# Performance work log

Measured on AMD Instinct MI355X. Metric: run time of the kernel, lower is better.

The kernel has to match this reference:

```python
import jax, jax.numpy as jnp
from jax import lax
import numpy as np

B, N, DIM = 2, 2048, 1024
HEADS, DIM_HEAD = 16, 64
KERNELS = (0, 3, 5, 7)
GROUPS = len(KERNELS)
HPG = HEADS // GROUPS          # heads per group = 4
CG = HPG * DIM_HEAD            # channels per group for depthwise conv = 256
INNER = HEADS * DIM_HEAD       # 1024


def _alibi_slopes(n):
    # power-of-2 branch of LearnedAlibiPosBias._get_slopes (n=4 here)
    start = 2.0 ** (-(2.0 ** -(np.log2(n) - 3)))
    return np.array([start * start ** i for i in range(n)], dtype=np.float32)


def setup_inputs() -> dict:
    key = jax.random.key(0)
    ks = jax.random.split(key, 24)
    d = {}
    d['x'] = jax.random.normal(ks[0], (B, N, DIM), jnp.float32)
    d['ln_gamma'] = jnp.ones((DIM,), jnp.float32)
    d['ln_beta'] = jnp.zeros((DIM,), jnp.float32)
    d['w_qkv'] = jax.random.normal(ks[1], (3 * INNER, DIM), jnp.float32) * 0.02
    i = 2
    for p in ('q', 'k', 'v'):
        for ksz in (3, 5, 7):
            d[f'dw{p}_w{ksz}'] = jax.random.normal(ks[i], (CG, 1, ksz), jnp.float32) * 0.1; i += 1
            d[f'dw{p}_b{ksz}'] = jax.random.normal(ks[i], (CG,), jnp.float32) * 0.02; i += 1
    # learned alibi slopes, initialized to the standard ALiBi values per group
    sl = _alibi_slopes(HPG).reshape(1, HPG, 1, 1)
    d['slopes'] = jnp.asarray(np.tile(sl, (GROUPS, 1, 1, 1)))
    d['w_out'] = jax.random.normal(ks[20], (DIM, INNER), jnp.float32) * 0.02
    return d


def _dw_causal_conv(xg, w, b, ksz):
    # xg: (B, CG, N); depthwise causal conv, left pad ksz-1
    xg = jnp.pad(xg, ((0, 0), (0, 0), (ksz - 1, 0)))
    out = lax.conv_general_dilated(xg, w, (1,), 'VALID',
                                   feature_group_count=CG,
                                   dimension_numbers=('NCH', 'OIH', 'NCH'))
    return out + b[None, :, None]


def _grouped_conv(t, w3, b3, w5, b5, w7, b7):
    # t: (B, INNER, N) channels laid out head-major; group g = channels [g*CG,(g+1)*CG)
    parts = [t[:, :CG]]  # group 0: kernel_size 0 -> Identity
    for i, (w, b, ksz) in enumerate(((w3, b3, 3), (w5, b5, 5), (w7, b7, 7))):
        parts.append(_dw_causal_conv(t[:, (i + 1) * CG:(i + 2) * CG], w, b, ksz))
    out = jnp.concatenate(parts, axis=1)                      # (B, INNER, N)
    out = out.reshape(B, HEADS, DIM_HEAD, N)
    return jnp.transpose(out, (0, 1, 3, 2))                   # (B, H, N, Dh)


def _forward(x, ln_gamma, ln_beta, w_qkv,
             dwq_w3, dwq_b3, dwq_w5, dwq_b5, dwq_w7, dwq_b7,
             dwk_w3, dwk_b3, dwk_w5, dwk_b5, dwk_w7, dwk_b7,
             dwv_w3, dwv_b3, dwv_w5, dwv_b5, dwv_w7, dwv_b7,
             slopes, w_out):
    scale = DIM_HEAD ** -0.5
    mu = jnp.mean(x, axis=-1, keepdims=True)
    var = jnp.var(x, axis=-1, keepdims=True)
    h = (x - mu) * lax.rsqrt(var + 1e-5) * ln_gamma + ln_beta   # (B, N, DIM)
    qkv = jnp.einsum('bnd,ed->ben', h, w_qkv)                   # (B, 3*INNER, N)
    q, k, v = jnp.split(qkv, 3, axis=1)
    q = _grouped_conv(q, dwq_w3, dwq_b3, dwq_w5, dwq_b5, dwq_w7, dwq_b7)
    k = _grouped_conv(k, dwk_w3, dwk_b3, dwk_w5, dwk_b5, dwk_w7, dwk_b7)
    v = _grouped_conv(v, dwv_w3, dwv_b3, dwv_w5, dwv_b5, dwv_w7, dwv_b7)
    sim = jnp.einsum('bhid,bhjd->bhij', q * scale, k)           # (B, H, N, N)
    idx = jnp.arange(N)
    dist = -jnp.abs(idx[None, :] - idx[:, None]).astype(sim.dtype)  # (N, N)
    bias = slopes.reshape(HEADS, 1, 1) * dist[None]             # (H, N, N)
    sim = sim + bias[None]
    causal = idx[None, :] > idx[:, None]                        # strictly future
    sim = jnp.where(causal[None, None], -jnp.finfo(sim.dtype).max, sim)
    attn = jax.nn.softmax(sim, axis=-1)
    out = jnp.einsum('bhij,bhjd->bhid', attn, v)                # (B, H, N, Dh)
    out = jnp.transpose(out, (0, 2, 1, 3)).reshape(B, N, INNER)
    return jnp.einsum('bne,de->bnd', out, w_out)


def reference(x, ln_gamma, ln_beta, w_qkv,
              dwq_w3, dwq_b3, dwq_w5, dwq_b5, dwq_w7, dwq_b7,
              dwk_w3, dwk_b3, dwk_w5, dwk_b5, dwk_w7, dwk_b7,
              dwv_w3, dwv_b3, dwv_w5, dwv_b5, dwv_w7, dwv_b7,
              slopes, w_out):
    return _forward(x, ln_gamma, ln_beta, w_qkv,
                    dwq_w3, dwq_b3, dwq_w5, dwq_b5, dwq_w7, dwq_b7,
                    dwk_w3, dwk_b3, dwk_w5, dwk_b5, dwk_w7, dwk_b7,
                    dwv_w3, dwv_b3, dwv_w5, dwv_b5, dwv_w7, dwv_b7,
                    slopes, w_out)
```

## Files before the change

kernel.cpp:

```cpp
#include <hip/hip_runtime.h>
#include <hip/hip_bf16.h>
#include <stdint.h>

typedef __bf16 bf8 __attribute__((ext_vector_type(8)));
typedef float  f4  __attribute__((ext_vector_type(4)));

constexpr int BATCH  = 2;
constexpr int SEQ    = 2048;
constexpr int DMODEL = 1024;
constexpr int NH     = 16;
constexpr int DHEAD  = 64;
constexpr int E3     = 3072;

static __device__ __forceinline__ f4 mfma16(bf8 a, bf8 b, f4 c){
  return __builtin_amdgcn_mfma_f32_16x16x32_bf16(a, b, c, 0, 0, 0);
}
static __device__ __forceinline__ uint32_t pack2(float a, float b){
  union { __bf16 h[2]; uint32_t u; } p;
  p.h[0] = (__bf16)a; p.h[1] = (__bf16)b;
  return p.u;
}
typedef const __attribute__((address_space(1))) uint32_t g_u32;
typedef __attribute__((address_space(3))) uint32_t l_u32;
static __device__ __forceinline__ void glds16(const __bf16* g, __bf16* l){
  __builtin_amdgcn_global_load_lds((g_u32*)g, (l_u32*)l, 16, 0, 0);
}

__global__ __launch_bounds__(256) void cvt_kernel(const float* __restrict__ s,
                                                  __bf16* __restrict__ d, int n){
  int i = (blockIdx.x * 256 + threadIdx.x) * 4;
  if(i < n){
    float4 v = *(const float4*)(s + i);
    __bf16 o[4] = {(__bf16)v.x, (__bf16)v.y, (__bf16)v.z, (__bf16)v.w};
    *(uint2*)(d + i) = *(const uint2*)o;
  }
}

__global__ __launch_bounds__(256) void prep_kernel(const float* __restrict__ x,
                                                   const float* __restrict__ gam,
                                                   const float* __restrict__ bet,
                                                   __bf16* __restrict__ h,
                                                   const float* __restrict__ wq,
                                                   __bf16* __restrict__ wqb){
  int bid = blockIdx.x;
  int tid = threadIdx.x;
  if(bid >= BATCH*SEQ){
    int i = ((bid - BATCH*SEQ) * 256 + tid) * 4;
    float4 v = *(const float4*)(wq + i);
    __bf16 o[4] = {(__bf16)v.x, (__bf16)v.y, (__bf16)v.z, (__bf16)v.w};
    *(uint2*)(wqb + i) = *(const uint2*)o;
    return;
  }
  int row = bid;
  const float* xr = x + (size_t)row * DMODEL;
  float4 v = *(const float4*)(xr + tid*4);
  float s = v.x + v.y + v.z + v.w;
  float ss = v.x*v.x + v.y*v.y + v.z*v.z + v.w*v.w;
#pragma unroll
  for(int m=1;m<64;m<<=1){ s += __shfl_xor(s, m); ss += __shfl_xor(ss, m); }
  __shared__ float sm[8];
  int wid = tid >> 6;
  if((tid & 63) == 0){ sm[wid] = s; sm[4+wid] = ss; }
  __syncthreads();
  s  = sm[0]+sm[1]+sm[2]+sm[3];
  ss = sm[4]+sm[5]+sm[6]+sm[7];
  float mu  = s * (1.f/DMODEL);
  float var = ss * (1.f/DMODEL) - mu*mu;
  float r = rsqrtf(var + 1e-5f);
  float4 g = *(const float4*)(gam + tid*4);
  float4 bb = *(const float4*)(bet + tid*4);
  __bf16 o[4] = { (__bf16)((v.x-mu)*r*g.x + bb.x), (__bf16)((v.y-mu)*r*g.y + bb.y),
                  (__bf16)((v.z-mu)*r*g.z + bb.z), (__bf16)((v.w-mu)*r*g.w + bb.w) };
  *(uint2*)(h + (size_t)row*DMODEL + tid*4) = *(uint2*)o;
}

template<typename CT>
__global__ __launch_bounds__(256) void gemm_nt(const __bf16* __restrict__ A,
                                               const __bf16* __restrict__ Bm,
                                               CT* __restrict__ C,
                                               int M, int Ncols, int K){
  __shared__ __align__(16) __bf16 sm[2*128*32];
  __bf16* As = sm;
  __bf16* Bs = sm + 128*32;
  int m0 = blockIdx.y * 128, n0 = blockIdx.x * 128;
  int tid = threadIdx.x;
  int lane = tid & 63, wid = tid >> 6;
  int quad = lane >> 4, l15 = lane & 15;
  int wm = (wid >> 1) * 64, wn = (wid & 1) * 64;
  f4 acc[4][4] = {};
  int r0 = wid*32 + (lane >> 2);
  int cofs = (lane & 3) * 8;
  const __bf16* ag = A  + (size_t)(m0 + r0) * K + cofs;
  const __bf16* bg = Bm + (size_t)(n0 + r0) * K + cofs;
  __bf16* asb0 = &As[(wid*32)*32];
  __bf16* asb1 = &As[(wid*32+16)*32];
  __bf16* bsb0 = &Bs[(wid*32)*32];
  __bf16* bsb1 = &Bs[(wid*32+16)*32];
  const size_t rowskip = (size_t)16 * K;
  for(int k0 = 0; k0 < K; k0 += 32){
    __syncthreads();
    glds16(ag + k0,           asb0);
    glds16(ag + rowskip + k0, asb1);
    glds16(bg + k0,           bsb0);
    glds16(bg + rowskip + k0, bsb1);
    __syncthreads();
    bf8 af[4], bfr[4];
#pragma unroll
    for(int i=0;i<4;i++){
      af[i]  = *(const bf8*)&As[(wm + i*16 + l15)*32 + quad*8];
      bfr[i] = *(const bf8*)&Bs[(wn + i*16 + l15)*32 + quad*8];
    }
#pragma unroll
    for(int mi=0;mi<4;mi++)
#pragma unroll
      for(int ni=0;ni<4;ni++)
        acc[mi][ni] = mfma16(af[mi], bfr[ni], acc[mi][ni]);
  }
  if constexpr (sizeof(CT) == 2){
    uint32_t* sp = (uint32_t*)sm;
#pragma unroll
    for(int qq=0; qq<4; qq++){
      __syncthreads();
      if((wid>>1) == (qq>>1)){
        int mi0 = (qq & 1) * 2;
#pragma unroll
        for(int mm=0; mm<2; mm++){
          int mi = mi0 + mm;
#pragma unroll
          for(int ni=0; ni<4; ni++)
#pragma unroll
            for(int r=0; r<4; r++){
              int lr = (mi - mi0)*16 + quad*4 + r;
              sm[lr*136 + wn + ni*16 + l15] = (__bf16)acc[mi][ni][r];
            }
        }
      }
      __syncthreads();
#pragma unroll
      for(int it=0; it<2; it++){
        int idx = it*256 + tid;
        int row = idx >> 4;
        int ck  = idx & 15;
        uint32_t o0 = sp[row*68 + ck*4 + 0];
        uint32_t o1 = sp[row*68 + ck*4 + 1];
        uint32_t o2 = sp[row*68 + ck*4 + 2];
        uint32_t o3 = sp[row*68 + ck*4 + 3];
        uint4 v = {o0, o1, o2, o3};
        *(uint4*)(C + (size_t)(m0 + qq*32 + row)*Ncols + n0 + ck*8) = v;
      }
    }
  } else {
#pragma unroll
    for(int mi=0;mi<4;mi++)
#pragma unroll
      for(int ni=0;ni<4;ni++)
#pragma unroll
        for(int r=0;r<4;r++){
          int row = m0 + wm + mi*16 + quad*4 + r;
          int col = n0 + wn + ni*16 + l15;
          C[(size_t)row*Ncols + col] = (CT)acc[mi][ni][r];
        }
  }
}

template<typename CT>
__global__ __launch_bounds__(256) void gemm_nt64(const __bf16* __restrict__ A,
                                                 const __bf16* __restrict__ Bm,
                                                 CT* __restrict__ C,
                                                 int M, int Ncols, int K){
  __shared__ __align__(16) __bf16 smb[(128+64)*32];
  __bf16* As = smb;
  __bf16* Bs = smb + 128*32;
  int m0 = blockIdx.y * 128, n0 = blockIdx.x * 64;
  int tid = threadIdx.x;
  int lane = tid & 63, wid = tid >> 6;
  int quad = lane >> 4, l15 = lane & 15;
  int wm = wid * 32;
  f4 acc[2][4] = {};
  int ra = wid*32 + (lane >> 2);
  int rb = wid*16 + (lane >> 2);
  int cofs = (lane & 3) * 8;
  const __bf16* ag = A  + (size_t)(m0 + ra) * K + cofs;
  const __bf16* bg = Bm + (size_t)(n0 + rb) * K + cofs;
  __bf16* asb0 = &As[(wid*32)*32];
  __bf16* asb1 = &As[(wid*32+16)*32];
  __bf16* bsb  = &Bs[(wid*16)*32];
  const size_t rowskip = (size_t)16 * K;
  for(int k0 = 0; k0 < K; k0 += 32){
    __syncthreads();
    glds16(ag + k0,           asb0);
    glds16(ag + rowskip + k0, asb1);
    glds16(bg + k0,           bsb);
    __syncthreads();
    bf8 af[2], bfr[4];
#pragma unroll
    for(int i=0;i<2;i++)
      af[i]  = *(const bf8*)&As[(wm + i*16 + l15)*32 + quad*8];
#pragma unroll
    for(int i=0;i<4;i++)
      bfr[i] = *(const bf8*)&Bs[(i*16 + l15)*32 + quad*8];
#pragma unroll
    for(int mi=0;mi<2;mi++)
#pragma unroll
      for(int ni=0;ni<4;ni++)
        acc[mi][ni] = mfma16(af[mi], bfr[ni], acc[mi][ni]);
  }
  if constexpr (sizeof(CT) == 4){
    float* sp = (float*)smb;
#pragma unroll
    for(int qq=0; qq<4; qq++){
      __syncthreads();
      if(wid == qq){
#pragma unroll
        for(int mi=0; mi<2; mi++)
#pragma unroll
          for(int ni=0; ni<4; ni++)
#pragma unroll
            for(int r=0; r<4; r++){
              int lr = mi*16 + quad*4 + r;
              sp[lr*68 + ni*16 + l15] = acc[mi][ni][r];
            }
      }
      __syncthreads();
#pragma unroll
      for(int it=0; it<2; it++){
        int idx = it*256 + tid;
        int row = idx >> 4;
        int ck  = idx & 15;
        float4 v = { sp[row*68 + ck*4 + 0], sp[row*68 + ck*4 + 1],
                     sp[row*68 + ck*4 + 2], sp[row*68 + ck*4 + 3] };
        *(float4*)(C + (size_t)(m0 + qq*32 + row)*Ncols + n0 + ck*4) = v;
      }
    }
  } else {
#pragma unroll
    for(int mi=0;mi<2;mi++)
#pragma unroll
      for(int ni=0;ni<4;ni++)
#pragma unroll
        for(int r=0;r<4;r++){
          int row = m0 + wm + mi*16 + quad*4 + r;
          int col = n0 + ni*16 + l15;
          C[(size_t)row*Ncols + col] = (CT)acc[mi][ni][r];
        }
  }
}

__global__ __launch_bounds__(256) void conv_kernel(const __bf16* __restrict__ qkv,
    __bf16* __restrict__ qo, __bf16* __restrict__ ko, __bf16* __restrict__ vt,
    const float* qw3,const float* qb3,const float* qw5,const float* qb5,const float* qw7,const float* qb7,
    const float* kw3,const float* kb3,const float* kw5,const float* kb5,const float* kw7,const float* kb7,
    const float* vw3,const float* vb3,const float* vw5,const float* vb5,const float* vw7,const float* vb7){
  __shared__ __align__(16) __bf16 tile[72*256];
  int nc = blockIdx.x;
  int ec = blockIdx.y;
  int b  = blockIdx.z;
  int tid = threadIdx.x;
  int n0 = nc * 64;
  {
    int rrow = tid >> 5;
    int ccol = (tid & 31) * 8;
    const __bf16* src = qkv + (size_t)b*SEQ*E3 + ec*256 + ccol;
#pragma unroll
    for(int p=0;p<9;p++){
      int row = p*8 + rrow;
      int n = n0 - 8 + row;
      uint4 v = {0u,0u,0u,0u};
      if(n >= 0) v = *(const uint4*)(src + (size_t)n*E3);
      *(uint4*)&tile[row*256 + ccol] = v;
    }
  }
  __syncthreads();
  int e = ec*256 + tid;
  int p  = e >> 10;
  int c  = e & 1023;
  int g  = c >> 8;
  int cg = c & 255;
  int hh = c >> 6;
  int dh = c & 63;
  const float* W[9]  = {qw3,qw5,qw7,kw3,kw5,kw7,vw3,vw5,vw7};
  const float* Bp[9] = {qb3,qb5,qb7,kb3,kb5,kb7,vb3,vb5,vb7};
  int ksz = (g==0)?0:((g==1)?3:((g==2)?5:7));
  float w[7] = {0,0,0,0,0,0,0};
  float bias = 0.f;
  if(g > 0){
    const float* wp = W[p*3 + g - 1];
    const float* bp = Bp[p*3 + g - 1];
    for(int t=0;t<ksz;t++) w[t] = wp[cg*ksz + t];
    bias = bp[cg];
  }
  float xh[6];
#pragma unroll
  for(int i=0;i<6;i++) xh[i] = (float)tile[(2+i)*256 + tid];
  if(p == 2){
    uint32_t vout[32];
#pragma unroll
    for(int blk=0; blk<8; blk++){
      __bf16 tmp[8];
#pragma unroll
      for(int u=0;u<8;u++){
        int dn = blk*8 + u;
        float cur = (float)tile[(8+dn)*256 + tid];
        float o;
        if(ksz == 0)      o = cur;
        else if(ksz == 3) o = w[0]*xh[4] + w[1]*xh[5] + w[2]*cur + bias;
        else if(ksz == 5) o = w[0]*xh[2] + w[1]*xh[3] + w[2]*xh[4] + w[3]*xh[5] + w[4]*cur + bias;
        else              o = w[0]*xh[0] + w[1]*xh[1] + w[2]*xh[2] + w[3]*xh[3] + w[4]*xh[4] + w[5]*xh[5] + w[6]*cur + bias;
        xh[0]=xh[1]; xh[1]=xh[2]; xh[2]=xh[3]; xh[3]=xh[4]; xh[4]=xh[5]; xh[5]=cur;
        tmp[u] = (__bf16)o;
      }
#pragma unroll
      for(int j=0;j<4;j++) vout[blk*4 + j] = ((const uint32_t*)tmp)[j];
    }
    __syncthreads();
    uint32_t* ot = (uint32_t*)tile;
#pragma unroll
    for(int j=0;j<32;j++) ot[tid*33 + j] = vout[j];
    __syncthreads();
#pragma unroll
    for(int it=0; it<8; it++){
      int idx = it*256 + tid;
      int ch  = idx >> 3;
      int ncq = idx & 7;
      uint32_t a0 = ot[ch*33 + ncq*4 + 0];
      uint32_t a1 = ot[ch*33 + ncq*4 + 1];
      uint32_t a2 = ot[ch*33 + ncq*4 + 2];
      uint32_t a3 = ot[ch*33 + ncq*4 + 3];
      uint4 val = {a0, a1, a2, a3};
      int hh2 = (ec & 3)*4 + (ch >> 6);
      int dh2 = ch & 63;
      *(uint4*)(vt + ((size_t)((b*NH + hh2)*DHEAD + dh2))*SEQ + n0 + ncq*8) = val;
    }
  } else {
    __bf16* outp = (p==0) ? qo : ko;
    __bf16* op = outp + ((size_t)(b*NH + hh)*SEQ)*DHEAD + dh;
#pragma unroll 4
    for(int dn=0; dn<64; dn++){
      float cur = (float)tile[(8+dn)*256 + tid];
      float o;
      if(ksz == 0)      o = cur;
      else if(ksz == 3) o = w[0]*xh[4] + w[1]*xh[5] + w[2]*cur + bias;
      else if(ksz == 5) o = w[0]*xh[2] + w[1]*xh[3] + w[2]*xh[4] + w[3]*xh[5] + w[4]*cur + bias;
      else              o = w[0]*xh[0] + w[1]*xh[1] + w[2]*xh[2] + w[3]*xh[3] + w[4]*xh[4] + w[5]*xh[5] + w[6]*cur + bias;
      xh[0]=xh[1]; xh[1]=xh[2]; xh[2]=xh[3]; xh[3]=xh[4]; xh[4]=xh[5]; xh[5]=cur;
      op[(size_t)(n0+dn)*DHEAD] = (__bf16)o;
    }
  }
}

__global__ __launch_bounds__(256, 2) void attn_kernel(const __bf16* __restrict__ Qin,
                                                      const __bf16* __restrict__ Kin,
                                                      const __bf16* __restrict__ Vtin,
                                                      const float* __restrict__ slopes,
                                                      __bf16* __restrict__ Oout){
  __shared__ __align__(16) __bf16 Ks[2][128*64];
  __shared__ __align__(16) __bf16 Vts[2][64*128];
  __shared__ __align__(16) __bf16 Ps[4][16*72];
  __shared__ float Al[4][16];
  int bid = blockIdx.x;
  int pr = bid >> 5;
  int by = (bid & 7) + ((bid >> 3) & 3) * 8;
  int b  = by >> 4, hh = by & 15;
  int tid = threadIdx.x, lane = tid & 63, w = tid >> 6;
  int quad = lane >> 4, l15 = lane & 15;
  const __bf16* qb  = Qin  + (size_t)by * SEQ * DHEAD;
  const __bf16* kb  = Kin  + (size_t)by * SEQ * DHEAD;
  const __bf16* vtb = Vtin + (size_t)by * DHEAD * SEQ;
  const float L2E = 1.4426950408889634f;
  float slope = slopes[hh];
  const float c1 = 0.125f * L2E;
  float c2 = slope * L2E;
  float c2_64 = c2 * 64.f;
  float cjb[16];
#pragma unroll
  for(int jt=0;jt<4;jt++)
#pragma unroll
    for(int r=0;r<4;r++)
      cjb[jt*4+r] = c2 * (float)(jt*16 + quad*4 + r);

  int sxq0 = ((quad     ^ (l15 & 7)) << 3);
  int sxq1 = (((quad+4) ^ (l15 & 7)) << 3);

  const __bf16* ksrc = kb + (size_t)(lane>>3)*DHEAD + ((lane&7) ^ ((lane>>3)&7))*8;
  const __bf16* vsrc[4];
#pragma unroll
  for(int u=0;u<4;u++){
    int g = w*4 + u;
    int vrow = g*4 + (lane>>4);
    vsrc[u] = vtb + (size_t)vrow*SEQ + (((lane&15) ^ (vrow&15)) * 8);
  }

  for(int ph=0; ph<2; ph++){
    int qi = ph ? (31 - pr) : pr;
    int q0 = qi * 64;
    int nst = (qi >> 1) + 1;
    int i0 = q0 + w*16;
    int i  = i0 + l15;
    bf8 aq0 = *(const bf8*)(qb + (size_t)i*DHEAD + quad*8);
    bf8 aq1 = *(const bf8*)(qb + (size_t)i*DHEAD + 32 + quad*8);
    f4 oacc[4] = {};
    float l_ = 0.f;
#pragma unroll
    for(int u=0;u<4;u++){
      int g = w*4 + u;
      glds16(ksrc + (size_t)g*8*DHEAD, &Ks[0][g*512]);
      glds16(vsrc[u],                  &Vts[0][g*512]);
    }
    __syncthreads();
    int cur = 0;
    for(int t=0; t<nst; t++){
      int j0 = t*128;
      bool pf = (t+1) < nst;
      if(pf){
        int nb = cur ^ 1;
#pragma unroll
        for(int u=0;u<4;u++){
          int g = w*4 + u;
          glds16(ksrc + (size_t)((t+1)*128 + g*8)*DHEAD, &Ks[nb][g*512]);
          glds16(vsrc[u] + (t+1)*128,                    &Vts[nb][g*512]);
        }
      }
      const __bf16* KsC  = Ks[cur];
      const __bf16* VtsC = Vts[cur];
      f4 s[8] = {};
      __builtin_amdgcn_s_setprio(1);
#pragma unroll
      for(int jt=0;jt<8;jt++){
        bf8 ak0 = *(const bf8*)&KsC[(jt*16+l15)*64 + sxq0];
        bf8 ak1 = *(const bf8*)&KsC[(jt*16+l15)*64 + sxq1];
        s[jt] = mfma16(ak0, aq0, s[jt]);
        s[jt] = mfma16(ak1, aq1, s[jt]);
      }
      __builtin_amdgcn_s_setprio(0);
      float lsum = 0.f;
      bool masked = (t == nst-1);
      float cdi = c2 * (float)(i - j0) + 8.0f;
#pragma unroll
      for(int h=0;h<2;h++){
        bf8 bv[2][4];
#pragma unroll
        for(int jj=0;jj<2;jj++){
          int jk = h*2 + jj;
#pragma unroll
          for(int nd=0;nd<4;nd++)
            bv[jj][nd] = *(const bf8*)&VtsC[(nd*16+l15)*128 + (((jk*4+quad) ^ l15) << 3)];
        }
        float sv[4][4];
        if(!masked){
#pragma unroll
          for(int jl=0;jl<4;jl++){
            int jt = h*4 + jl;
#pragma unroll
            for(int r=0;r<4;r++)
              sv[jl][r] = fmaf(s[jt][r], c1, cjb[jl*4+r] - cdi + (h ? c2_64 : 0.f));
          }
        } else {
#pragma unroll
          for(int jl=0;jl<4;jl++){
            int jt = h*4 + jl;
#pragma unroll
            for(int r=0;r<4;r++){
              int j = j0 + jt*16 + quad*4 + r;
              int d = i - j;
              float val = fmaf(s[jt][r], c1, -fmaf(c2, (float)d, 8.0f));
              sv[jl][r] = (d < 0) ? -1e30f : val;
            }
          }
        }
#pragma unroll
        for(int jl=0;jl<4;jl++){
          float p0 = __builtin_amdgcn_exp2f(sv[jl][0]);
          float p1 = __builtin_amdgcn_exp2f(sv[jl][1]);
          float p2 = __builtin_amdgcn_exp2f(sv[jl][2]);
          float p3 = __builtin_amdgcn_exp2f(sv[jl][3]);
          lsum += (p0+p1)+(p2+p3);
          uint2 pk = { pack2(p0,p1), pack2(p2,p3) };
          *(uint2*)&Ps[w][l15*72 + jl*16 + quad*4] = pk;
        }
        __builtin_amdgcn_s_setprio(1);
#pragma unroll
        for(int jj=0;jj<2;jj++){
          bf8 ap = *(const bf8*)&Ps[w][l15*72 + jj*32 + quad*8];
#pragma unroll
          for(int nd=0;nd<4;nd++)
            oacc[nd] = mfma16(ap, bv[jj][nd], oacc[nd]);
        }
        __builtin_amdgcn_s_setprio(0);
      }
      lsum += __shfl_xor(lsum, 16);
      lsum += __shfl_xor(lsum, 32);
      l_ += lsum;
      __syncthreads();
      cur ^= 1;
    }
    if(quad == 0) Al[w][l15] = 1.0f / l_;
    f4 linv = *(const f4*)&Al[w][quad*4];
#pragma unroll
    for(int nd=0;nd<4;nd++)
#pragma unroll
      for(int r=0;r<4;r++){
        int io = i0 + quad*4 + r;
        Oout[((size_t)(b*SEQ + io))*DMODEL + hh*64 + nd*16 + l15] =
            (__bf16)(oacc[nd][r] * linv[r]);
      }
    if(ph == 0) __syncthreads();
  }
}

extern "C" void kernel_launch(void* const* d_in, const int* in_sizes, int n_in,
                              void* d_out, int out_size, void* d_ws, size_t ws_size,
                              hipStream_t stream){
  const float* x      = (const float*)d_in[0];
  const float* gam    = (const float*)d_in[1];
  const float* bet    = (const float*)d_in[2];
  const float* w_qkv  = (const float*)d_in[3];
  const float* slopes = (const float*)d_in[22];
  const float* w_out  = (const float*)d_in[23];
  float* out = (float*)d_out;

  char* ws = (char*)d_ws;
  __bf16* h       = (__bf16*)(ws);
  __bf16* qpost   = (__bf16*)(ws);
  __bf16* qkv     = (__bf16*)(ws + ((size_t)8  << 20));
  __bf16* att     = (__bf16*)(ws + ((size_t)8  << 20));
  __bf16* wout_bf = (__bf16*)(ws + ((size_t)24 << 20));
  __bf16* wqkv_bf = (__bf16*)(ws + ((size_t)32 << 20));
  __bf16* kpost   = (__bf16*)(ws + ((size_t)32 << 20));
  __bf16* vtp     = (__bf16*)(ws + ((size_t)40 << 20));

  constexpr int NQKV = 3 * DMODEL * DMODEL;
  constexpr int NOUT = DMODEL * DMODEL;

  prep_kernel<<<BATCH*SEQ + NQKV/4/256, 256, 0, stream>>>(x, gam, bet, h, w_qkv, wqkv_bf);
  gemm_nt<__bf16><<<dim3(E3/128, (BATCH*SEQ)/128), 256, 0, stream>>>(
      h, wqkv_bf, qkv, BATCH*SEQ, E3, DMODEL);
  conv_kernel<<<dim3(32, 12, BATCH), 256, 0, stream>>>(qkv, qpost, kpost, vtp,
    (const float*)d_in[4],(const float*)d_in[5],(const float*)d_in[6],(const float*)d_in[7],
    (const float*)d_in[8],(const float*)d_in[9],
    (const float*)d_in[10],(const float*)d_in[11],(const float*)d_in[12],(const float*)d_in[13],
    (const float*)d_in[14],(const float*)d_in[15],
    (const float*)d_in[16],(const float*)d_in[17],(const float*)d_in[18],(const float*)d_in[19],
    (const float*)d_in[20],(const float*)d_in[21]);
  cvt_kernel<<<NOUT/4/256, 256, 0, stream>>>(w_out, wout_bf, NOUT);
  attn_kernel<<<dim3(512), 256, 0, stream>>>(qpost, kpost, vtp, slopes, att);
  gemm_nt64<float><<<dim3(DMODEL/64, (BATCH*SEQ)/128), 256, 0, stream>>>(
      att, wout_bf, out, BATCH*SEQ, DMODEL, DMODEL);
}
```

Measured before the change: 241.6 us.

## Double-buffer GEMM LDS loads and fold w_out conversion into attention launch

Both GEMM kernels now use two LDS buffers, so the next K-slice is prefetched with global_load_lds while MFMAs run on the current one, and only one barrier is needed per iteration. The separate w_out fp32-to-bf16 conversion kernel is removed; the attention launch gets 1024 extra blocks that do the conversion and exit early. The aim is to hide global load latency in the GEMMs and save one kernel launch. The cost is twice the LDS in the GEMMs, which may lower occupancy, and extra trailing blocks scheduled in the attention grid.

Result: no change. 238.2 us (-1.4%).

```diff
diff --git a/kernel.cpp b/kernel.cpp
--- a/kernel.cpp
+++ b/kernel.cpp
@@ -24,16 +24,6 @@
 typedef __attribute__((address_space(3))) uint32_t l_u32;
 static __device__ __forceinline__ void glds16(const __bf16* g, __bf16* l){
   __builtin_amdgcn_global_load_lds((g_u32*)g, (l_u32*)l, 16, 0, 0);
-}
-
-__global__ __launch_bounds__(256) void cvt_kernel(const float* __restrict__ s,
-                                                  __bf16* __restrict__ d, int n){
-  int i = (blockIdx.x * 256 + threadIdx.x) * 4;
-  if(i < n){
-    float4 v = *(const float4*)(s + i);
-    __bf16 o[4] = {(__bf16)v.x, (__bf16)v.y, (__bf16)v.z, (__bf16)v.w};
-    *(uint2*)(d + i) = *(const uint2*)o;
-  }
 }
 
 __global__ __launch_bounds__(256) void prep_kernel(const float* __restrict__ x,
@@ -79,9 +69,8 @@
                                                const __bf16* __restrict__ Bm,
                                                CT* __restrict__ C,
                                                int M, int Ncols, int K){
-  __shared__ __align__(16) __bf16 sm[2*128*32];
-  __bf16* As = sm;
-  __bf16* Bs = sm + 128*32;
+  __shared__ __align__(16) __bf16 As[2][128*32];
+  __shared__ __align__(16) __bf16 Bs[2][128*32];
   int m0 = blockIdx.y * 128, n0 = blockIdx.x * 128;
   int tid = threadIdx.x;
   int lane = tid & 63, wid = tid >> 6;
@@ -92,32 +81,42 @@
   int cofs = (lane & 3) * 8;
   const __bf16* ag = A  + (size_t)(m0 + r0) * K + cofs;
   const __bf16* bg = Bm + (size_t)(n0 + r0) * K + cofs;
-  __bf16* asb0 = &As[(wid*32)*32];
-  __bf16* asb1 = &As[(wid*32+16)*32];
-  __bf16* bsb0 = &Bs[(wid*32)*32];
-  __bf16* bsb1 = &Bs[(wid*32+16)*32];
+  const int d0 = (wid*32)*32, d1 = (wid*32+16)*32;
   const size_t rowskip = (size_t)16 * K;
+  glds16(ag,           &As[0][d0]);
+  glds16(ag + rowskip, &As[0][d1]);
+  glds16(bg,           &Bs[0][d0]);
+  glds16(bg + rowskip, &Bs[0][d1]);
+  __syncthreads();
+  int cur = 0;
   for(int k0 = 0; k0 < K; k0 += 32){
-    __syncthreads();
-    glds16(ag + k0,           asb0);
-    glds16(ag + rowskip + k0, asb1);
-    glds16(bg + k0,           bsb0);
-    glds16(bg + rowskip + k0, bsb1);
-    __syncthreads();
+    int k1 = k0 + 32;
+    if(k1 < K){
+      int nb = cur ^ 1;
+      glds16(ag + k1,           &As[nb][d0]);
+      glds16(ag + rowskip + k1, &As[nb][d1]);
+      glds16(bg + k1,           &Bs[nb][d0]);
+      glds16(bg + rowskip + k1, &Bs[nb][d1]);
+    }
+    const __bf16* AsC = As[cur];
+    const __bf16* BsC = Bs[cur];
     bf8 af[4], bfr[4];
 #pragma unroll
     for(int i=0;i<4;i++){
-      af[i]  = *(const bf8*)&As[(wm + i*16 + l15)*32 + quad*8];
-      bfr[i] = *(const bf8*)&Bs[(wn + i*16 + l15)*32 + quad*8];
+      af[i]  = *(const bf8*)&AsC[(wm + i*16 + l15)*32 + quad*8];
+      bfr[i] = *(const bf8*)&BsC[(wn + i*16 + l15)*32 + quad*8];
     }
 #pragma unroll
     for(int mi=0;mi<4;mi++)
 #pragma unroll
       for(int ni=0;ni<4;ni++)
         acc[mi][ni] = mfma16(af[mi], bfr[ni], acc[mi][ni]);
+    __syncthreads();
+    cur ^= 1;
   }
   if constexpr (sizeof(CT) == 2){
-    uint32_t* sp = (uint32_t*)sm;
+    __bf16* scr = (__bf16*)As;
+    uint32_t* sp = (uint32_t*)As;
 #pragma unroll
     for(int qq=0; qq<4; qq++){
       __syncthreads();
@@ -131,7 +130,7 @@
 #pragma unroll
             for(int r=0; r<4; r++){
               int lr = (mi - mi0)*16 + quad*4 + r;
-              sm[lr*136 + wn + ni*16 + l15] = (__bf16)acc[mi][ni][r];
+              scr[lr*136 + wn + ni*16 + l15] = (__bf16)acc[mi][ni][r];
             }
         }
       }
@@ -168,9 +167,8 @@
                                                  const __bf16* __restrict__ Bm,
                                                  CT* __restrict__ C,
                                                  int M, int Ncols, int K){
-  __shared__ __align__(16) __bf16 smb[(128+64)*32];
-  __bf16* As = smb;
-  __bf16* Bs = smb + 128*32;
+  __shared__ __align__(16) __bf16 As[2][128*32];
+  __shared__ __align__(16) __bf16 Bs[2][64*32];
   int m0 = blockIdx.y * 128, n0 = blockIdx.x * 64;
   int tid = threadIdx.x;
   int lane = tid & 63, wid = tid >> 6;
@@ -182,31 +180,40 @@
   int cofs = (lane & 3) * 8;
   const __bf16* ag = A  + (size_t)(m0 + ra) * K + cofs;
   const __bf16* bg = Bm + (size_t)(n0 + rb) * K + cofs;
-  __bf16* asb0 = &As[(wid*32)*32];
-  __bf16* asb1 = &As[(wid*32+16)*32];
-  __bf16* bsb  = &Bs[(wid*16)*32];
+  const int da0 = (wid*32)*32, da1 = (wid*32+16)*32, db = (wid*16)*32;
   const size_t rowskip = (size_t)16 * K;
+  glds16(ag,           &As[0][da0]);
+  glds16(ag + rowskip, &As[0][da1]);
+  glds16(bg,           &Bs[0][db]);
+  __syncthreads();
+  int cur = 0;
   for(int k0 = 0; k0 < K; k0 += 32){
-    __syncthreads();
-    glds16(ag + k0,           asb0);
-    glds16(ag + rowskip + k0, asb1);
-    glds16(bg + k0,           bsb);
-    __syncthreads();
+    int k1 = k0 + 32;
+    if(k1 < K){
+      int nb = cur ^ 1;
+      glds16(ag + k1,           &As[nb][da0]);
+      glds16(ag + rowskip + k1, &As[nb][da1]);
+      glds16(bg + k1,           &Bs[nb][db]);
+    }
+    const __bf16* AsC = As[cur];
+    const __bf16* BsC = Bs[cur];
     bf8 af[2], bfr[4];
 #pragma unroll
     for(int i=0;i<2;i++)
-      af[i]  = *(const bf8*)&As[(wm + i*16 + l15)*32 + quad*8];
+      af[i]  = *(const bf8*)&AsC[(wm + i*16 + l15)*32 + quad*8];
 #pragma unroll
     for(int i=0;i<4;i++)
-      bfr[i] = *(const bf8*)&Bs[(i*16 + l15)*32 + quad*8];
+      bfr[i] = *(const bf8*)&BsC[(i*16 + l15)*32 + quad*8];
 #pragma unroll
     for(int mi=0;mi<2;mi++)
 #pragma unroll
       for(int ni=0;ni<4;ni++)
         acc[mi][ni] = mfma16(af[mi], bfr[ni], acc[mi][ni]);
+    __syncthreads();
+    cur ^= 1;
   }
   if constexpr (sizeof(CT) == 4){
-    float* sp = (float*)smb;
+    float* sp = (float*)As;
 #pragma unroll
     for(int qq=0; qq<4; qq++){
       __syncthreads();
@@ -352,16 +359,26 @@
                                                       const __bf16* __restrict__ Kin,
                                                       const __bf16* __restrict__ Vtin,
                                                       const float* __restrict__ slopes,
-                                                      __bf16* __restrict__ Oout){
+                                                      __bf16* __restrict__ Oout,
+                                                      const float* __restrict__ wsrc,
+                                                      __bf16* __restrict__ wdst){
   __shared__ __align__(16) __bf16 Ks[2][128*64];
   __shared__ __align__(16) __bf16 Vts[2][64*128];
   __shared__ __align__(16) __bf16 Ps[4][16*72];
   __shared__ float Al[4][16];
   int bid = blockIdx.x;
+  int tid = threadIdx.x;
+  if(bid >= 512){
+    int i = ((bid - 512) * 256 + tid) * 4;
+    float4 v = *(const float4*)(wsrc + i);
+    __bf16 o[4] = {(__bf16)v.x, (__bf16)v.y, (__bf16)v.z, (__bf16)v.w};
+    *(uint2*)(wdst + i) = *(const uint2*)o;
+    return;
+  }
   int pr = bid >> 5;
   int by = (bid & 7) + ((bid >> 3) & 3) * 8;
   int b  = by >> 4, hh = by & 15;
-  int tid = threadIdx.x, lane = tid & 63, w = tid >> 6;
+  int lane = tid & 63, w = tid >> 6;
   int quad = lane >> 4, l15 = lane & 15;
   const __bf16* qb  = Qin  + (size_t)by * SEQ * DHEAD;
   const __bf16* kb  = Kin  + (size_t)by * SEQ * DHEAD;
@@ -529,7 +546,6 @@
   __bf16* vtp     = (__bf16*)(ws + ((size_t)40 << 20));
 
   constexpr int NQKV = 3 * DMODEL * DMODEL;
-  constexpr int NOUT = DMODEL * DMODEL;
 
   prep_kernel<<<BATCH*SEQ + NQKV/4/256, 256, 0, stream>>>(x, gam, bet, h, w_qkv, wqkv_bf);
   gemm_nt<__bf16><<<dim3(E3/128, (BATCH*SEQ)/128), 256, 0, stream>>>(
@@ -541,8 +557,8 @@
     (const float*)d_in[14],(const float*)d_in[15],
     (const float*)d_in[16],(const float*)d_in[17],(const float*)d_in[18],(const float*)d_in[19],
     (const float*)d_in[20],(const float*)d_in[21]);
-  cvt_kernel<<<NOUT/4/256, 256, 0, stream>>>(w_out, wout_bf, NOUT);
-  attn_kernel<<<dim3(512), 256, 0, stream>>>(qpost, kpost, vtp, slopes, att);
+  attn_kernel<<<dim3(1536), 256, 0, stream>>>(qpost, kpost, vtp, slopes, att,
+                                              w_out, wout_bf);
   gemm_nt64<float><<<dim3(DMODEL/64, (BATCH*SEQ)/128), 256, 0, stream>>>(
       att, wout_bf, out, BATCH*SEQ, DMODEL, DMODEL);
 }
```
